# Kernel tuning notes

Measured on AMD Instinct MI355X. Metric: run time of the kernel, lower is better.

Reference implementation:

```python
import jax, jax.numpy as jnp
import numpy as np

NUM_HEADS = 16

def setup_inputs() -> dict:
    key = jax.random.key(0)
    ks = jax.random.split(key, 9)
    E = 1024
    T, B = 2048, 2
    s = E ** -0.5
    return {
        "query": jax.random.normal(ks[0], (T, B, E), dtype=jnp.float32),
        "Wq": jax.random.normal(ks[1], (E, E), dtype=jnp.float32) * s,
        "bq": jax.random.normal(ks[2], (E,), dtype=jnp.float32) * 0.02,
        "Wk": jax.random.normal(ks[3], (E, E), dtype=jnp.float32) * s,
        "bk": jax.random.normal(ks[4], (E,), dtype=jnp.float32) * 0.02,
        "Wv": jax.random.normal(ks[5], (E, E), dtype=jnp.float32) * s,
        "bv": jax.random.normal(ks[6], (E,), dtype=jnp.float32) * 0.02,
        "Wo": jax.random.normal(ks[7], (E, E), dtype=jnp.float32) * s,
        "bo": jax.random.normal(ks[8], (E,), dtype=jnp.float32) * 0.02,
    }

def reference(query, Wq, bq, Wk, bk, Wv, bv, Wo, bo):
    # query: [T, B, E] (seq-first, fairseq/ESM layout)
    T, B, E = query.shape
    H = NUM_HEADS
    D = E // H
    scaling = D ** -0.5
    # projections (eqx Linear: x @ W.T + b); note k/v also come from `query` (self-attention)
    q = (query @ Wq.T + bq) * scaling
    k = query @ Wk.T + bk
    v = query @ Wv.T + bv
    # [T, B, E] -> [B*H, T, D]
    q = q.reshape(T, B * H, D).transpose(1, 0, 2)
    k = k.reshape(T, B * H, D).transpose(1, 0, 2)
    v = v.reshape(T, B * H, D).transpose(1, 0, 2)
    # full score matrix [B*H, T, T], softmax in fp32 (as in original)
    scores = jnp.einsum('ntd,nsd->nts', q, k)
    attn_w = jax.nn.softmax(scores.astype(jnp.float32), axis=-1)
    attn = jnp.einsum('nts,nsd->ntd', attn_w.astype(v.dtype), v)
    # [B*H, T, D] -> [T, B, E]
    attn = attn.transpose(1, 0, 2).reshape(T, B, E)
    return attn @ Wo.T + bo
```

## Files before the change

kernel.cpp:

```cpp
#include <hip/hip_runtime.h>
#include <hip/hip_bf16.h>


typedef __attribute__((ext_vector_type(8))) short short8;
typedef __attribute__((ext_vector_type(4))) float f32x4;
typedef __attribute__((ext_vector_type(16))) float f32x16;
typedef __attribute__((ext_vector_type(4))) unsigned u32x4;

#define T_DIM 2048
#define B_DIM 2
#define E_DIM 1024
#define H_DIM 16
#define D_DIM 64
#define M_ROWS (T_DIM * B_DIM)
#define QKV_N (3 * E_DIM)
#define HEAD_ELEMS (32 * 2048 * 64)
#define LOG2E 1.44269504088896340736f

__device__ __forceinline__ unsigned short f2bf(float f) {
    unsigned u = __builtin_bit_cast(unsigned, f);
    unsigned r = (u + 0x7fffu + ((u >> 16) & 1u)) >> 16;
    return (unsigned short)r;
}

__device__ __forceinline__ unsigned cvt_pk_bf16(float lo, float hi) {
    unsigned d;
    asm("v_cvt_pk_bf16_f32 %0, %1, %2" : "=v"(d) : "v"(lo), "v"(hi));
    return d;
}

__device__ __forceinline__ void gload_lds16(const void* g, void* l) {
    __builtin_amdgcn_global_load_lds(
        (const __attribute__((address_space(1))) void*)g,
        (__attribute__((address_space(3))) void*)l, 16, 0, 0);
}

__device__ __forceinline__ f32x16 mfma32(short8 a, short8 b, f32x16 c) {
    return __builtin_amdgcn_mfma_f32_32x32x16_bf16(a, b, c, 0, 0, 0);
}

__global__ __launch_bounds__(256) void cast_all(
    const float* __restrict__ X,
    const float* __restrict__ Wq, const float* __restrict__ Wk,
    const float* __restrict__ Wv, const float* __restrict__ Wo,
    unsigned short* __restrict__ Xbf,
    unsigned short* __restrict__ Wcat,
    unsigned short* __restrict__ Wobf)
{
    int idx = blockIdx.x * 256 + threadIdx.x;
    size_t base = (size_t)idx * 8;
    int row = (int)(base >> 10);
    int col = (int)(base & 1023);
    const float* src;
    unsigned short* dst;
    float scale = 1.0f;
    if (row < 4096) {
        src = X + base;
        dst = Xbf + base;
    } else if (row < 7168) {
        int wrow = row - 4096;
        if (wrow < 1024)      { src = Wq + ((size_t)wrow << 10) + col; scale = 0.125f * LOG2E; }
        else if (wrow < 2048) { src = Wk + ((size_t)(wrow - 1024) << 10) + col; }
        else                  { src = Wv + ((size_t)(wrow - 2048) << 10) + col; }
        dst = Wcat + ((size_t)wrow << 10) + col;
    } else {
        int wrow = row - 7168;
        src = Wo + ((size_t)wrow << 10) + col;
        dst = Wobf + ((size_t)wrow << 10) + col;
    }
    float4 f0 = *(const float4*)src;
    float4 f1 = *(const float4*)(src + 4);
    short8 r;
    r[0] = (short)f2bf(f0.x * scale);
    r[1] = (short)f2bf(f0.y * scale);
    r[2] = (short)f2bf(f0.z * scale);
    r[3] = (short)f2bf(f0.w * scale);
    r[4] = (short)f2bf(f1.x * scale);
    r[5] = (short)f2bf(f1.y * scale);
    r[6] = (short)f2bf(f1.z * scale);
    r[7] = (short)f2bf(f1.w * scale);
    *(short8*)dst = r;
}

__global__ __launch_bounds__(256) void bias_fuse(
    const float* __restrict__ bq, const float* __restrict__ bk,
    const float* __restrict__ bv, float* __restrict__ biasq)
{
    int i = blockIdx.x * 256 + threadIdx.x;
    if (i < 1024)       biasq[i] = 0.125f * LOG2E * bq[i];
    else if (i < 2048)  biasq[i] = bk[i - 1024];
    else if (i < 3072)  biasq[i] = bv[i - 2048];
}

template <int MODE>
__global__ __launch_bounds__(256) void gemm_bt(
    const unsigned short* __restrict__ A,
    const unsigned short* __restrict__ B,
    const float* __restrict__ bias,
    void* __restrict__ outp,
    int M, int N, int K)
{
    __shared__ alignas(16) unsigned short As[2][128 * 32];
    __shared__ alignas(16) unsigned short Bs[2][128 * 32];
    const int tid = threadIdx.x;
    const int wave = tid >> 6, lane = tid & 63;
    const int lr = lane & 15, lg = lane >> 4;
    const int nbx = N >> 7;
    const int bx = blockIdx.x % nbx, by = blockIdx.x / nbx;
    const int wr = wave >> 1, wc = wave & 1;

    f32x4 acc[4][4] = {};

    auto stage = [&](int buf, int kt) {
#pragma unroll
        for (int pass = 0; pass < 2; ++pass) {
            int c = pass * 256 + wave * 64 + lane;
            int row = c >> 2, kc = c & 3;
            gload_lds16(A + (size_t)(by * 128 + row) * K + kt + kc * 8,
                        (char*)&As[buf][0] + c * 16);
            gload_lds16(B + (size_t)(bx * 128 + row) * K + kt + kc * 8,
                        (char*)&Bs[buf][0] + c * 16);
        }
    };

    const int NK = K >> 5;
    stage(0, 0);
    for (int ki = 0; ki < NK; ++ki) {
        const int buf = ki & 1;
        if (ki < NK - 1) {
            stage(buf ^ 1, (ki + 1) * 32);
            asm volatile("s_waitcnt vmcnt(4)" ::: "memory");
        } else {
            asm volatile("s_waitcnt vmcnt(0)" ::: "memory");
        }
        __builtin_amdgcn_s_barrier();
        __builtin_amdgcn_sched_barrier(0);

        short8 af[4], bf[4];
#pragma unroll
        for (int m = 0; m < 4; ++m)
            af[m] = *(const short8*)&As[buf][(wr * 64 + m * 16 + lr) * 32 + lg * 8];
#pragma unroll
        for (int n = 0; n < 4; ++n)
            bf[n] = *(const short8*)&Bs[buf][(wc * 64 + n * 16 + lr) * 32 + lg * 8];
        __builtin_amdgcn_s_setprio(1);
#pragma unroll
        for (int m = 0; m < 4; ++m)
#pragma unroll
            for (int n = 0; n < 4; ++n)
                acc[m][n] = __builtin_amdgcn_mfma_f32_16x16x32_bf16(af[m], bf[n], acc[m][n], 0, 0, 0);
        __builtin_amdgcn_s_setprio(0);

        asm volatile("s_waitcnt lgkmcnt(0)" ::: "memory");
        __builtin_amdgcn_sched_barrier(0);
        __builtin_amdgcn_s_barrier();
    }

    const int gcol0 = bx * 128 + wc * 64;
    const int grow0 = by * 128 + wr * 64;
    if (MODE == 0) {
        unsigned short* qb = (unsigned short*)outp;
#pragma unroll
        for (int m = 0; m < 4; ++m) {
#pragma unroll
            for (int n = 0; n < 4; ++n) {
                int col = gcol0 + n * 16 + lr;
                float bsv = bias[col];
                int which = col >> 10;
                int e = col & 1023;
                int h = e >> 6, d = e & 63;
                if (which < 2) {
                    unsigned short* bufb = qb + (size_t)which * HEAD_ELEMS;
#pragma unroll
                    for (int j = 0; j < 4; ++j) {
                        int r = grow0 + m * 16 + lg * 4 + j;
                        int t = r >> 1, b = r & 1;
                        int bh = b * 16 + h;
                        bufb[((size_t)bh * 2048 + t) * 64 + d] = f2bf(acc[m][n][j] + bsv);
                    }
                } else {
                    unsigned* vT32 = (unsigned*)(qb + (size_t)2 * HEAD_ELEMS);
                    int t0 = (grow0 + m * 16 + lg * 4) >> 1;
                    int dwidx = t0 >> 1;
                    int dwp = (dwidx & ~6) | ((dwidx & 2) << 1) | ((dwidx & 4) >> 1);
                    unsigned w0 = (unsigned)f2bf(acc[m][n][0] + bsv) |
                                  ((unsigned)f2bf(acc[m][n][2] + bsv) << 16);
                    unsigned w1 = (unsigned)f2bf(acc[m][n][1] + bsv) |
                                  ((unsigned)f2bf(acc[m][n][3] + bsv) << 16);
                    vT32[(size_t)(h * 64 + d) * 1024 + dwp] = w0;
                    vT32[(size_t)((16 + h) * 64 + d) * 1024 + dwp] = w1;
                }
            }
        }
    } else {
        float* O = (float*)outp;
#pragma unroll
        for (int m = 0; m < 4; ++m) {
#pragma unroll
            for (int n = 0; n < 4; ++n) {
                int col = gcol0 + n * 16 + lr;
                float bsv = bias[col];
#pragma unroll
                for (int j = 0; j < 4; ++j) {
                    int r = grow0 + m * 16 + lg * 4 + j;
                    O[(size_t)r * N + col] = acc[m][n][j] + bsv;
                }
            }
        }
    }
}

struct AttnCtx {
    const unsigned short* kh;
    const unsigned short* vh;
    int tid, ql, hi;
};

template<bool DO_PV>
__device__ __forceinline__ void attn_step(
    const AttnCtx& cx, int t,
    unsigned short (*Ks)[64 * 64], unsigned short (*Vs)[64 * 64],
    const short8 (&qv)[4],
    const short8 (&vfP)[8], const short8 (&paP)[4],
    short8 (&vfC)[8], short8 (&paC)[4],
    f32x16 (&accO)[2], float& lrun)
{
    const int buf = t & 1;
    const int tid = cx.tid, ql = cx.ql, hi = cx.hi;
    if (t < 31) {
        const int kt = (t + 1) * 64;
#pragma unroll
        for (int p = 0; p < 2; ++p) {
            int c = p * 256 + tid;
            int row = c >> 3;
            int sxb = ((c & 7) * 16) ^ ((row & 7) << 4);
            gload_lds16(cx.kh + (size_t)(kt + row) * 64 + (sxb >> 1),
                        (char*)&Ks[buf ^ 1][0] + c * 16);
        }
#pragma unroll
        for (int p = 0; p < 2; ++p) {
            int c = p * 256 + tid;
            int d = c >> 3;
            int sxb = ((c & 7) * 16) ^ ((d & 7) << 4);
            gload_lds16(cx.vh + (size_t)d * 2048 + kt + (sxb >> 1),
                        (char*)&Vs[buf ^ 1][0] + c * 16);
        }
        asm volatile("s_waitcnt vmcnt(4)" ::: "memory");
    } else {
        asm volatile("s_waitcnt vmcnt(0)" ::: "memory");
    }
    __builtin_amdgcn_s_barrier();
    __builtin_amdgcn_sched_barrier(0);

    const char* Kb = (const char*)&Ks[buf][0];
    const char* Vb = (const char*)&Vs[buf][0];

    f32x16 st[2] = {};
    __builtin_amdgcn_s_setprio(1);
#pragma unroll
    for (int m = 0; m < 2; ++m) {
        int krow = m * 32 + ql;
#pragma unroll
        for (int c = 0; c < 4; ++c) {
            int bo = (krow * 128 + c * 32 + hi * 16) ^ ((krow & 7) << 4);
            short8 ka = *(const short8*)(Kb + bo);
            st[m] = mfma32(ka, qv[c], st[m]);
        }
    }
#pragma unroll
    for (int n = 0; n < 2; ++n) {
        int d = n * 32 + ql;
#pragma unroll
        for (int kc = 0; kc < 4; ++kc) {
            int bo = (d * 128 + kc * 32 + hi * 16) ^ ((d & 7) << 4);
            vfC[n * 4 + kc] = *(const short8*)(Vb + bo);
        }
    }
    if constexpr (DO_PV) {
#pragma unroll
        for (int n = 0; n < 2; ++n)
#pragma unroll
            for (int kc = 0; kc < 4; ++kc)
                accO[n] = mfma32(vfP[n * 4 + kc], paP[kc], accO[n]);
    }
    __builtin_amdgcn_s_setprio(0);
    __builtin_amdgcn_sched_barrier(0);

    float rs = 0.0f;
#pragma unroll
    for (int m = 0; m < 2; ++m)
#pragma unroll
        for (int r = 0; r < 16; ++r) {
            float e = __builtin_amdgcn_exp2f(st[m][r]);
            st[m][r] = e;
            rs += e;
        }
    lrun += rs;

#pragma unroll
    for (int kc = 0; kc < 4; ++kc) {
        int m = kc >> 1, b8 = (kc & 1) * 8;
        u32x4 u;
        u[0] = cvt_pk_bf16(st[m][b8 + 0], st[m][b8 + 1]);
        u[1] = cvt_pk_bf16(st[m][b8 + 2], st[m][b8 + 3]);
        u[2] = cvt_pk_bf16(st[m][b8 + 4], st[m][b8 + 5]);
        u[3] = cvt_pk_bf16(st[m][b8 + 6], st[m][b8 + 7]);
        paC[kc] = __builtin_bit_cast(short8, u);
    }

    asm volatile("s_waitcnt lgkmcnt(0)" ::: "memory");
    __builtin_amdgcn_sched_barrier(0);
    __builtin_amdgcn_s_barrier();
}

__global__ __launch_bounds__(256, 2) void attn_fwd(
    const unsigned short* __restrict__ q,
    const unsigned short* __restrict__ k,
    const unsigned short* __restrict__ vT,
    unsigned short* __restrict__ outb)
{
    __shared__ alignas(16) unsigned short Ks[2][64 * 64];
    __shared__ alignas(16) unsigned short Vs[2][64 * 64];
    const int tid = threadIdx.x, wv = tid >> 6, l = tid & 63;
    const int ql = l & 31, hi = l >> 5;
    const int lid = blockIdx.x;
    const int xcd = lid & 7, slot = lid >> 3;
    const int bh = xcd * 4 + (slot >> 4);
    const int q0 = (slot & 15) * 128;
    const unsigned short* qh = q + (size_t)bh * (2048 * 64);
    AttnCtx cx;
    cx.kh = k + (size_t)bh * (2048 * 64);
    cx.vh = vT + (size_t)bh * (64 * 2048);
    cx.tid = tid; cx.ql = ql; cx.hi = hi;

    const int qrow = q0 + wv * 32 + ql;
    short8 qv[4];
#pragma unroll
    for (int c = 0; c < 4; ++c)
        qv[c] = *(const short8*)&qh[(size_t)qrow * 64 + c * 16 + hi * 8];

    f32x16 accO[2] = {};
    float lrun = 0.0f;
    short8 vfA[8], vfB[8], paA[4], paB[4];

    {
#pragma unroll
        for (int p = 0; p < 2; ++p) {
            int c = p * 256 + tid;
            int row = c >> 3;
            int sxb = ((c & 7) * 16) ^ ((row & 7) << 4);
            gload_lds16(cx.kh + (size_t)row * 64 + (sxb >> 1),
                        (char*)&Ks[0][0] + c * 16);
        }
#pragma unroll
        for (int p = 0; p < 2; ++p) {
            int c = p * 256 + tid;
            int d = c >> 3;
            int sxb = ((c & 7) * 16) ^ ((d & 7) << 4);
            gload_lds16(cx.vh + (size_t)d * 2048 + (sxb >> 1),
                        (char*)&Vs[0][0] + c * 16);
        }
    }

    attn_step<false>(cx, 0, Ks, Vs, qv, vfB, paB, vfA, paA, accO, lrun);
    for (int t = 1; t < 31; t += 2) {
        attn_step<true>(cx, t,     Ks, Vs, qv, vfA, paA, vfB, paB, accO, lrun);
        attn_step<true>(cx, t + 1, Ks, Vs, qv, vfB, paB, vfA, paA, accO, lrun);
    }
    attn_step<true>(cx, 31, Ks, Vs, qv, vfA, paA, vfB, paB, accO, lrun);
#pragma unroll
    for (int n = 0; n < 2; ++n)
#pragma unroll
        for (int kc = 0; kc < 4; ++kc)
            accO[n] = mfma32(vfB[n * 4 + kc], paB[kc], accO[n]);

    const float ltot = lrun + __shfl_xor(lrun, 32);
    const float inv = 1.0f / ltot;
    const int b = bh >> 4, h = bh & 15;
    const int orow = qrow * 2 + b;
#pragma unroll
    for (int n = 0; n < 2; ++n)
#pragma unroll
        for (int rq = 0; rq < 4; ++rq) {
            uint2 u;
            u.x = cvt_pk_bf16(accO[n][rq * 4 + 0] * inv, accO[n][rq * 4 + 1] * inv);
            u.y = cvt_pk_bf16(accO[n][rq * 4 + 2] * inv, accO[n][rq * 4 + 3] * inv);
            *(uint2*)&outb[(size_t)orow * 1024 + h * 64 + n * 32 + rq * 8 + hi * 4] = u;
        }
}

extern "C" void kernel_launch(void* const* d_in, const int* in_sizes, int n_in,
                              void* d_out, int out_size, void* d_ws, size_t ws_size,
                              hipStream_t stream) {
    const float* X  = (const float*)d_in[0];
    const float* Wq = (const float*)d_in[1];
    const float* bq = (const float*)d_in[2];
    const float* Wk = (const float*)d_in[3];
    const float* bk = (const float*)d_in[4];
    const float* Wv = (const float*)d_in[5];
    const float* bv = (const float*)d_in[6];
    const float* Wo = (const float*)d_in[7];
    const float* bo = (const float*)d_in[8];
    float* out = (float*)d_out;

    char* ws = (char*)d_ws;
    if (ws_size < ((size_t)49 << 20)) return;
    unsigned short* Xbf   = (unsigned short*)(ws);
    unsigned short* Wcat  = (unsigned short*)(ws + ((size_t)8  << 20));
    unsigned short* Wobf  = (unsigned short*)(ws + ((size_t)14 << 20));
    unsigned short* qb    = (unsigned short*)(ws + ((size_t)16 << 20));
    unsigned short* ab    = (unsigned short*)(ws + ((size_t)40 << 20));
    float*          biasq = (float*)(ws + ((size_t)48 << 20));
    unsigned short* kb  = qb + (size_t)HEAD_ELEMS;
    unsigned short* vTb = qb + (size_t)2 * HEAD_ELEMS;

    cast_all<<<4096, 256, 0, stream>>>(X, Wq, Wk, Wv, Wo, Xbf, Wcat, Wobf);
    bias_fuse<<<12, 256, 0, stream>>>(bq, bk, bv, biasq);
    gemm_bt<0><<<dim3((M_ROWS / 128) * (QKV_N / 128)), 256, 0, stream>>>(
        Xbf, Wcat, biasq, (void*)qb, M_ROWS, QKV_N, E_DIM);
    attn_fwd<<<dim3(32 * 16), 256, 0, stream>>>(qb, kb, vTb, ab);
    gemm_bt<1><<<dim3((M_ROWS / 128) * (E_DIM / 128)), 256, 0, stream>>>(
        ab, Wobf, bo, (void*)out, M_ROWS, E_DIM, E_DIM);
}
```

Before: 117.4 us.

## Double KV tile to 128 keys per stage to halve barriers

Each pipeline stage of the attention kernel now loads 128 keys of K and V into LDS instead of 64, and processes them as two 64-key sub-steps between a single pair of barriers. This halves the number of block-wide barriers and vmcnt waits per head. LDS use doubles to 64 KB per block, which may limit occupancy at two blocks per CU. The exp2/rowsum loop also uses four independent accumulators to shorten the dependency chain.

```diff
diff --git a/kernel.cpp b/kernel.cpp
--- a/kernel.cpp
+++ b/kernel.cpp
@@ -217,49 +217,20 @@
 };
 
 template<bool DO_PV>
-__device__ __forceinline__ void attn_step(
-    const AttnCtx& cx, int t,
-    unsigned short (*Ks)[64 * 64], unsigned short (*Vs)[64 * 64],
+__device__ __forceinline__ void attn_sub(
+    const AttnCtx& cx, int sub, const char* Kb, const char* Vb,
     const short8 (&qv)[4],
     const short8 (&vfP)[8], const short8 (&paP)[4],
     short8 (&vfC)[8], short8 (&paC)[4],
     f32x16 (&accO)[2], float& lrun)
 {
-    const int buf = t & 1;
-    const int tid = cx.tid, ql = cx.ql, hi = cx.hi;
-    if (t < 31) {
-        const int kt = (t + 1) * 64;
-#pragma unroll
-        for (int p = 0; p < 2; ++p) {
-            int c = p * 256 + tid;
-            int row = c >> 3;
-            int sxb = ((c & 7) * 16) ^ ((row & 7) << 4);
-            gload_lds16(cx.kh + (size_t)(kt + row) * 64 + (sxb >> 1),
-                        (char*)&Ks[buf ^ 1][0] + c * 16);
-        }
-#pragma unroll
-        for (int p = 0; p < 2; ++p) {
-            int c = p * 256 + tid;
-            int d = c >> 3;
-            int sxb = ((c & 7) * 16) ^ ((d & 7) << 4);
-            gload_lds16(cx.vh + (size_t)d * 2048 + kt + (sxb >> 1),
-                        (char*)&Vs[buf ^ 1][0] + c * 16);
-        }
-        asm volatile("s_waitcnt vmcnt(4)" ::: "memory");
-    } else {
-        asm volatile("s_waitcnt vmcnt(0)" ::: "memory");
-    }
-    __builtin_amdgcn_s_barrier();
-    __builtin_amdgcn_sched_barrier(0);
-
-    const char* Kb = (const char*)&Ks[buf][0];
-    const char* Vb = (const char*)&Vs[buf][0];
+    const int ql = cx.ql, hi = cx.hi;
 
     f32x16 st[2] = {};
     __builtin_amdgcn_s_setprio(1);
 #pragma unroll
     for (int m = 0; m < 2; ++m) {
-        int krow = m * 32 + ql;
+        int krow = sub * 64 + m * 32 + ql;
 #pragma unroll
         for (int c = 0; c < 4; ++c) {
             int bo = (krow * 128 + c * 32 + hi * 16) ^ ((krow & 7) << 4);
@@ -272,7 +243,7 @@
         int d = n * 32 + ql;
 #pragma unroll
         for (int kc = 0; kc < 4; ++kc) {
-            int bo = (d * 128 + kc * 32 + hi * 16) ^ ((d & 7) << 4);
+            int bo = (d * 256 + sub * 128 + kc * 32 + hi * 16) ^ ((d & 7) << 4);
             vfC[n * 4 + kc] = *(const short8*)(Vb + bo);
         }
     }
@@ -286,16 +257,21 @@
     __builtin_amdgcn_s_setprio(0);
     __builtin_amdgcn_sched_barrier(0);
 
-    float rs = 0.0f;
-#pragma unroll
-    for (int m = 0; m < 2; ++m)
-#pragma unroll
-        for (int r = 0; r < 16; ++r) {
-            float e = __builtin_amdgcn_exp2f(st[m][r]);
-            st[m][r] = e;
-            rs += e;
-        }
-    lrun += rs;
+    float rs0 = 0.f, rs1 = 0.f, rs2 = 0.f, rs3 = 0.f;
+#pragma unroll
+    for (int m = 0; m < 2; ++m) {
+#pragma unroll
+        for (int r = 0; r < 16; r += 4) {
+            float e0 = __builtin_amdgcn_exp2f(st[m][r + 0]);
+            float e1 = __builtin_amdgcn_exp2f(st[m][r + 1]);
+            float e2 = __builtin_amdgcn_exp2f(st[m][r + 2]);
+            float e3 = __builtin_amdgcn_exp2f(st[m][r + 3]);
+            st[m][r + 0] = e0; st[m][r + 1] = e1;
+            st[m][r + 2] = e2; st[m][r + 3] = e3;
+            rs0 += e0; rs1 += e1; rs2 += e2; rs3 += e3;
+        }
+    }
+    lrun += (rs0 + rs1) + (rs2 + rs3);
 
 #pragma unroll
     for (int kc = 0; kc < 4; ++kc) {
@@ -307,10 +283,6 @@
         u[3] = cvt_pk_bf16(st[m][b8 + 6], st[m][b8 + 7]);
         paC[kc] = __builtin_bit_cast(short8, u);
     }
-
-    asm volatile("s_waitcnt lgkmcnt(0)" ::: "memory");
-    __builtin_amdgcn_sched_barrier(0);
-    __builtin_amdgcn_s_barrier();
 }
 
 __global__ __launch_bounds__(256, 2) void attn_fwd(
@@ -319,8 +291,8 @@
     const unsigned short* __restrict__ vT,
     unsigned short* __restrict__ outb)
 {
-    __shared__ alignas(16) unsigned short Ks[2][64 * 64];
-    __shared__ alignas(16) unsigned short Vs[2][64 * 64];
+    __shared__ alignas(16) unsigned short Ks[2][128 * 64];
+    __shared__ alignas(16) unsigned short Vs[2][64 * 128];
     const int tid = threadIdx.x, wv = tid >> 6, l = tid & 63;
     const int ql = l & 31, hi = l >> 5;
     const int lid = blockIdx.x;
@@ -343,31 +315,52 @@
     float lrun = 0.0f;
     short8 vfA[8], vfB[8], paA[4], paB[4];
 
-    {
-#pragma unroll
-        for (int p = 0; p < 2; ++p) {
+    auto stage = [&](int buf, int kt) {
+#pragma unroll
+        for (int p = 0; p < 4; ++p) {
             int c = p * 256 + tid;
             int row = c >> 3;
             int sxb = ((c & 7) * 16) ^ ((row & 7) << 4);
-            gload_lds16(cx.kh + (size_t)row * 64 + (sxb >> 1),
-                        (char*)&Ks[0][0] + c * 16);
-        }
-#pragma unroll
-        for (int p = 0; p < 2; ++p) {
+            gload_lds16(cx.kh + (size_t)(kt + row) * 64 + (sxb >> 1),
+                        (char*)&Ks[buf][0] + c * 16);
+        }
+#pragma unroll
+        for (int p = 0; p < 4; ++p) {
             int c = p * 256 + tid;
-            int d = c >> 3;
-            int sxb = ((c & 7) * 16) ^ ((d & 7) << 4);
-            gload_lds16(cx.vh + (size_t)d * 2048 + (sxb >> 1),
-                        (char*)&Vs[0][0] + c * 16);
-        }
-    }
-
-    attn_step<false>(cx, 0, Ks, Vs, qv, vfB, paB, vfA, paA, accO, lrun);
-    for (int t = 1; t < 31; t += 2) {
-        attn_step<true>(cx, t,     Ks, Vs, qv, vfA, paA, vfB, paB, accO, lrun);
-        attn_step<true>(cx, t + 1, Ks, Vs, qv, vfB, paB, vfA, paA, accO, lrun);
-    }
-    attn_step<true>(cx, 31, Ks, Vs, qv, vfA, paA, vfB, paB, accO, lrun);
+            int d = c >> 4;
+            int sxb = ((c & 15) * 16) ^ ((d & 7) << 4);
+            gload_lds16(cx.vh + (size_t)d * 2048 + kt + (sxb >> 1),
+                        (char*)&Vs[buf][0] + c * 16);
+        }
+    };
+
+    stage(0, 0);
+    for (int ki = 0; ki < 16; ++ki) {
+        const int buf = ki & 1;
+        if (ki < 15) {
+            stage(buf ^ 1, (ki + 1) * 128);
+            asm volatile("s_waitcnt vmcnt(8)" ::: "memory");
+        } else {
+            asm volatile("s_waitcnt vmcnt(0)" ::: "memory");
+        }
+        __builtin_amdgcn_s_barrier();
+        __builtin_amdgcn_sched_barrier(0);
+
+        const char* Kb = (const char*)&Ks[buf][0];
+        const char* Vb = (const char*)&Vs[buf][0];
+
+        if (ki == 0) {
+            attn_sub<false>(cx, 0, Kb, Vb, qv, vfB, paB, vfA, paA, accO, lrun);
+            attn_sub<true >(cx, 1, Kb, Vb, qv, vfA, paA, vfB, paB, accO, lrun);
+        } else {
+            attn_sub<true>(cx, 0, Kb, Vb, qv, vfB, paB, vfA, paA, accO, lrun);
+            attn_sub<true>(cx, 1, Kb, Vb, qv, vfA, paA, vfB, paB, accO, lrun);
+        }
+
+        asm volatile("s_waitcnt lgkmcnt(0)" ::: "memory");
+        __builtin_amdgcn_sched_barrier(0);
+        __builtin_amdgcn_s_barrier();
+    }
 #pragma unroll
     for (int n = 0; n < 2; ++n)
 #pragma unroll
```

Measured after the change: 118.5 us. No clear change (+1.0%).

## Use triple-buffered LDS pipelines with one barrier per step in GEMM and attention

Applied to the files above, without the earlier changes.

Both the projection GEMM and the attention kernel move from double to triple buffering in LDS (attention uses 3 K slots and 4 V slots), prefetching two tiles ahead. Each iteration now needs only one barrier instead of two. Attention no longer keeps V fragments in registers across steps; it reads the previous step's V from LDS at PV time. The exp-sum loop is split into four partial accumulators. This adds LDS usage, which may reduce occupancy, and complicates slot indexing.

```diff
diff --git a/kernel.cpp b/kernel.cpp
--- a/kernel.cpp
+++ b/kernel.cpp
@@ -100,8 +100,8 @@
     void* __restrict__ outp,
     int M, int N, int K)
 {
-    __shared__ alignas(16) unsigned short As[2][128 * 32];
-    __shared__ alignas(16) unsigned short Bs[2][128 * 32];
+    __shared__ alignas(16) unsigned short As[3][128 * 32];
+    __shared__ alignas(16) unsigned short Bs[3][128 * 32];
     const int tid = threadIdx.x;
     const int wave = tid >> 6, lane = tid & 63;
     const int lr = lane & 15, lg = lane >> 4;
@@ -111,38 +111,40 @@
 
     f32x4 acc[4][4] = {};
 
-    auto stage = [&](int buf, int kt) {
+    auto stage = [&](int slot, int kt) {
 #pragma unroll
         for (int pass = 0; pass < 2; ++pass) {
             int c = pass * 256 + wave * 64 + lane;
             int row = c >> 2, kc = c & 3;
             gload_lds16(A + (size_t)(by * 128 + row) * K + kt + kc * 8,
-                        (char*)&As[buf][0] + c * 16);
+                        (char*)&As[slot][0] + c * 16);
             gload_lds16(B + (size_t)(bx * 128 + row) * K + kt + kc * 8,
-                        (char*)&Bs[buf][0] + c * 16);
+                        (char*)&Bs[slot][0] + c * 16);
         }
     };
 
     const int NK = K >> 5;
     stage(0, 0);
+    stage(1, 32);
+    int s3 = 0;
     for (int ki = 0; ki < NK; ++ki) {
-        const int buf = ki & 1;
-        if (ki < NK - 1) {
-            stage(buf ^ 1, (ki + 1) * 32);
-            asm volatile("s_waitcnt vmcnt(4)" ::: "memory");
-        } else {
-            asm volatile("s_waitcnt vmcnt(0)" ::: "memory");
-        }
+        asm volatile("s_waitcnt lgkmcnt(0)" ::: "memory");
+        if (ki < NK - 1) asm volatile("s_waitcnt vmcnt(4)" ::: "memory");
+        else             asm volatile("s_waitcnt vmcnt(0)" ::: "memory");
         __builtin_amdgcn_s_barrier();
         __builtin_amdgcn_sched_barrier(0);
+        if (ki + 2 < NK) {
+            int ns = s3 + 2; if (ns >= 3) ns -= 3;
+            stage(ns, (ki + 2) * 32);
+        }
 
         short8 af[4], bf[4];
 #pragma unroll
         for (int m = 0; m < 4; ++m)
-            af[m] = *(const short8*)&As[buf][(wr * 64 + m * 16 + lr) * 32 + lg * 8];
+            af[m] = *(const short8*)&As[s3][(wr * 64 + m * 16 + lr) * 32 + lg * 8];
 #pragma unroll
         for (int n = 0; n < 4; ++n)
-            bf[n] = *(const short8*)&Bs[buf][(wc * 64 + n * 16 + lr) * 32 + lg * 8];
+            bf[n] = *(const short8*)&Bs[s3][(wc * 64 + n * 16 + lr) * 32 + lg * 8];
         __builtin_amdgcn_s_setprio(1);
 #pragma unroll
         for (int m = 0; m < 4; ++m)
@@ -151,9 +153,7 @@
                 acc[m][n] = __builtin_amdgcn_mfma_f32_16x16x32_bf16(af[m], bf[n], acc[m][n], 0, 0, 0);
         __builtin_amdgcn_s_setprio(0);
 
-        asm volatile("s_waitcnt lgkmcnt(0)" ::: "memory");
-        __builtin_amdgcn_sched_barrier(0);
-        __builtin_amdgcn_s_barrier();
+        s3 = (s3 + 1 == 3) ? 0 : s3 + 1;
     }
 
     const int gcol0 = bx * 128 + wc * 64;
@@ -216,44 +216,37 @@
     int tid, ql, hi;
 };
 
-template<bool DO_PV>
+template<bool DO_PV, bool DO_STAGE, bool LASTWAIT>
 __device__ __forceinline__ void attn_step(
-    const AttnCtx& cx, int t,
-    unsigned short (*Ks)[64 * 64], unsigned short (*Vs)[64 * 64],
+    const AttnCtx& cx, int kt_next,
+    const char* Kb, const char* Vprv, char* Kst, char* Vst,
     const short8 (&qv)[4],
-    const short8 (&vfP)[8], const short8 (&paP)[4],
-    short8 (&vfC)[8], short8 (&paC)[4],
+    const short8 (&paP)[4], short8 (&paC)[4],
     f32x16 (&accO)[2], float& lrun)
 {
-    const int buf = t & 1;
     const int tid = cx.tid, ql = cx.ql, hi = cx.hi;
-    if (t < 31) {
-        const int kt = (t + 1) * 64;
+    asm volatile("s_waitcnt lgkmcnt(0)" ::: "memory");
+    if constexpr (LASTWAIT) asm volatile("s_waitcnt vmcnt(0)" ::: "memory");
+    else                    asm volatile("s_waitcnt vmcnt(4)" ::: "memory");
+    __builtin_amdgcn_s_barrier();
+    __builtin_amdgcn_sched_barrier(0);
+
+    if constexpr (DO_STAGE) {
 #pragma unroll
         for (int p = 0; p < 2; ++p) {
             int c = p * 256 + tid;
             int row = c >> 3;
             int sxb = ((c & 7) * 16) ^ ((row & 7) << 4);
-            gload_lds16(cx.kh + (size_t)(kt + row) * 64 + (sxb >> 1),
-                        (char*)&Ks[buf ^ 1][0] + c * 16);
+            gload_lds16(cx.kh + (size_t)(kt_next + row) * 64 + (sxb >> 1), Kst + c * 16);
         }
 #pragma unroll
         for (int p = 0; p < 2; ++p) {
             int c = p * 256 + tid;
             int d = c >> 3;
             int sxb = ((c & 7) * 16) ^ ((d & 7) << 4);
-            gload_lds16(cx.vh + (size_t)d * 2048 + kt + (sxb >> 1),
-                        (char*)&Vs[buf ^ 1][0] + c * 16);
-        }
-        asm volatile("s_waitcnt vmcnt(4)" ::: "memory");
-    } else {
-        asm volatile("s_waitcnt vmcnt(0)" ::: "memory");
-    }
-    __builtin_amdgcn_s_barrier();
-    __builtin_amdgcn_sched_barrier(0);
-
-    const char* Kb = (const char*)&Ks[buf][0];
-    const char* Vb = (const char*)&Vs[buf][0];
+            gload_lds16(cx.vh + (size_t)d * 2048 + kt_next + (sxb >> 1), Vst + c * 16);
+        }
+    }
 
     f32x16 st[2] = {};
     __builtin_amdgcn_s_setprio(1);
@@ -267,35 +260,36 @@
             st[m] = mfma32(ka, qv[c], st[m]);
         }
     }
-#pragma unroll
-    for (int n = 0; n < 2; ++n) {
-        int d = n * 32 + ql;
-#pragma unroll
-        for (int kc = 0; kc < 4; ++kc) {
-            int bo = (d * 128 + kc * 32 + hi * 16) ^ ((d & 7) << 4);
-            vfC[n * 4 + kc] = *(const short8*)(Vb + bo);
-        }
-    }
     if constexpr (DO_PV) {
 #pragma unroll
-        for (int n = 0; n < 2; ++n)
-#pragma unroll
-            for (int kc = 0; kc < 4; ++kc)
-                accO[n] = mfma32(vfP[n * 4 + kc], paP[kc], accO[n]);
+        for (int n = 0; n < 2; ++n) {
+            int d = n * 32 + ql;
+#pragma unroll
+            for (int kc = 0; kc < 4; ++kc) {
+                int bo = (d * 128 + kc * 32 + hi * 16) ^ ((d & 7) << 4);
+                short8 va = *(const short8*)(Vprv + bo);
+                accO[n] = mfma32(va, paP[kc], accO[n]);
+            }
+        }
     }
     __builtin_amdgcn_s_setprio(0);
     __builtin_amdgcn_sched_barrier(0);
 
-    float rs = 0.0f;
-#pragma unroll
-    for (int m = 0; m < 2; ++m)
-#pragma unroll
-        for (int r = 0; r < 16; ++r) {
-            float e = __builtin_amdgcn_exp2f(st[m][r]);
-            st[m][r] = e;
-            rs += e;
-        }
-    lrun += rs;
+    float rs0 = 0.f, rs1 = 0.f, rs2 = 0.f, rs3 = 0.f;
+#pragma unroll
+    for (int m = 0; m < 2; ++m) {
+#pragma unroll
+        for (int r = 0; r < 16; r += 4) {
+            float e0 = __builtin_amdgcn_exp2f(st[m][r + 0]);
+            float e1 = __builtin_amdgcn_exp2f(st[m][r + 1]);
+            float e2 = __builtin_amdgcn_exp2f(st[m][r + 2]);
+            float e3 = __builtin_amdgcn_exp2f(st[m][r + 3]);
+            st[m][r + 0] = e0; st[m][r + 1] = e1;
+            st[m][r + 2] = e2; st[m][r + 3] = e3;
+            rs0 += e0; rs1 += e1; rs2 += e2; rs3 += e3;
+        }
+    }
+    lrun += (rs0 + rs1) + (rs2 + rs3);
 
 #pragma unroll
     for (int kc = 0; kc < 4; ++kc) {
@@ -307,10 +301,6 @@
         u[3] = cvt_pk_bf16(st[m][b8 + 6], st[m][b8 + 7]);
         paC[kc] = __builtin_bit_cast(short8, u);
     }
-
-    asm volatile("s_waitcnt lgkmcnt(0)" ::: "memory");
-    __builtin_amdgcn_sched_barrier(0);
-    __builtin_amdgcn_s_barrier();
 }
 
 __global__ __launch_bounds__(256, 2) void attn_fwd(
@@ -319,8 +309,8 @@
     const unsigned short* __restrict__ vT,
     unsigned short* __restrict__ outb)
 {
-    __shared__ alignas(16) unsigned short Ks[2][64 * 64];
-    __shared__ alignas(16) unsigned short Vs[2][64 * 64];
+    __shared__ alignas(16) unsigned short Ks[3][64 * 64];
+    __shared__ alignas(16) unsigned short Vs[4][64 * 64];
     const int tid = threadIdx.x, wv = tid >> 6, l = tid & 63;
     const int ql = l & 31, hi = l >> 5;
     const int lid = blockIdx.x;
@@ -333,6 +323,9 @@
     cx.vh = vT + (size_t)bh * (64 * 2048);
     cx.tid = tid; cx.ql = ql; cx.hi = hi;
 
+#define KSLOT(i) ((char*)&Ks[i][0])
+#define VSLOT(i) ((char*)&Vs[i][0])
+
     const int qrow = q0 + wv * 32 + ql;
     short8 qv[4];
 #pragma unroll
@@ -341,38 +334,74 @@
 
     f32x16 accO[2] = {};
     float lrun = 0.0f;
-    short8 vfA[8], vfB[8], paA[4], paB[4];
-
-    {
+    short8 paA[4], paB[4];
+
+#pragma unroll
+    for (int tt = 0; tt < 2; ++tt) {
 #pragma unroll
         for (int p = 0; p < 2; ++p) {
             int c = p * 256 + tid;
             int row = c >> 3;
             int sxb = ((c & 7) * 16) ^ ((row & 7) << 4);
-            gload_lds16(cx.kh + (size_t)row * 64 + (sxb >> 1),
-                        (char*)&Ks[0][0] + c * 16);
+            gload_lds16(cx.kh + (size_t)(tt * 64 + row) * 64 + (sxb >> 1),
+                        KSLOT(tt) + c * 16);
         }
 #pragma unroll
         for (int p = 0; p < 2; ++p) {
             int c = p * 256 + tid;
             int d = c >> 3;
             int sxb = ((c & 7) * 16) ^ ((d & 7) << 4);
-            gload_lds16(cx.vh + (size_t)d * 2048 + (sxb >> 1),
-                        (char*)&Vs[0][0] + c * 16);
-        }
-    }
-
-    attn_step<false>(cx, 0, Ks, Vs, qv, vfB, paB, vfA, paA, accO, lrun);
-    for (int t = 1; t < 31; t += 2) {
-        attn_step<true>(cx, t,     Ks, Vs, qv, vfA, paA, vfB, paB, accO, lrun);
-        attn_step<true>(cx, t + 1, Ks, Vs, qv, vfB, paB, vfA, paA, accO, lrun);
-    }
-    attn_step<true>(cx, 31, Ks, Vs, qv, vfA, paA, vfB, paB, accO, lrun);
-#pragma unroll
-    for (int n = 0; n < 2; ++n)
-#pragma unroll
-        for (int kc = 0; kc < 4; ++kc)
-            accO[n] = mfma32(vfB[n * 4 + kc], paB[kc], accO[n]);
+            gload_lds16(cx.vh + (size_t)d * 2048 + tt * 64 + (sxb >> 1),
+                        VSLOT(tt) + c * 16);
+        }
+    }
+
+    int k3 = 0, v4 = 0;
+    auto adv = [&]() { k3 = (k3 + 1 == 3) ? 0 : k3 + 1; v4 = (v4 + 1) & 3; };
+
+    attn_step<false, true, false>(cx, 2 * 64, KSLOT(0), nullptr,
+                                  KSLOT(2), VSLOT(2),
+                                  qv, paB, paA, accO, lrun);
+    adv();
+    for (int t = 1; t <= 27; t += 2) {
+        int ns3 = (k3 + 2 >= 3) ? k3 - 1 : k3 + 2;
+        attn_step<true, true, false>(cx, (t + 2) * 64,
+                                     KSLOT(k3), VSLOT((v4 + 3) & 3),
+                                     KSLOT(ns3), VSLOT((v4 + 2) & 3),
+                                     qv, paA, paB, accO, lrun);
+        adv();
+        ns3 = (k3 + 2 >= 3) ? k3 - 1 : k3 + 2;
+        attn_step<true, true, false>(cx, (t + 3) * 64,
+                                     KSLOT(k3), VSLOT((v4 + 3) & 3),
+                                     KSLOT(ns3), VSLOT((v4 + 2) & 3),
+                                     qv, paB, paA, accO, lrun);
+        adv();
+    }
+    {
+        int ns3 = (k3 + 2 >= 3) ? k3 - 1 : k3 + 2;
+        attn_step<true, true, false>(cx, 31 * 64,
+                                     KSLOT(k3), VSLOT((v4 + 3) & 3),
+                                     KSLOT(ns3), VSLOT((v4 + 2) & 3),
+                                     qv, paA, paB, accO, lrun);
+        adv();
+    }
+    attn_step<true, false, false>(cx, 0, KSLOT(k3), VSLOT((v4 + 3) & 3),
+                                  nullptr, nullptr,
+                                  qv, paB, paA, accO, lrun);
+    adv();
+    attn_step<true, false, true>(cx, 0, KSLOT(k3), VSLOT((v4 + 3) & 3),
+                                 nullptr, nullptr,
+                                 qv, paA, paB, accO, lrun);
+#pragma unroll
+    for (int n = 0; n < 2; ++n) {
+        int d = n * 32 + ql;
+#pragma unroll
+        for (int kc = 0; kc < 4; ++kc) {
+            int bo = (d * 128 + kc * 32 + hi * 16) ^ ((d & 7) << 4);
+            short8 va = *(const short8*)(VSLOT(3) + bo);
+            accO[n] = mfma32(va, paB[kc], accO[n]);
+        }
+    }
 
     const float ltot = lrun + __shfl_xor(lrun, 32);
     const float inv = 1.0f / ltot;
@@ -387,6 +416,8 @@
             u.y = cvt_pk_bf16(accO[n][rq * 4 + 2] * inv, accO[n][rq * 4 + 3] * inv);
             *(uint2*)&outb[(size_t)orow * 1024 + h * 64 + n * 32 + rq * 8 + hi * 4] = u;
         }
+#undef KSLOT
+#undef VSLOT
 }
 
 extern "C" void kernel_launch(void* const* d_in, const int* in_sizes, int n_in,
```

Result: no change. 119.4 us (+1.7%).
